# Optimization experiments

Measured on AMD Instinct MI355X. Metric: run time of the kernel, lower is better.

## Reference

```python
import jax, jax.numpy as jnp
import numpy as np

SEQ = 4096
E = 2048

def setup_inputs() -> dict:
    key = jax.random.key(0)
    kx, kq, kk, kv = jax.random.split(key, 4)
    scale = 1.0 / np.sqrt(E)
    x = jax.random.normal(kx, (SEQ, E), dtype=jnp.float32)
    # nn.Linear weights: shape [out, in], applied as x @ W.T
    Wq = jax.random.uniform(kq, (E, E), dtype=jnp.float32, minval=-scale, maxval=scale)
    Wk = jax.random.uniform(kk, (E, E), dtype=jnp.float32, minval=-scale, maxval=scale)
    Wv = jax.random.uniform(kv, (E, E), dtype=jnp.float32, minval=-scale, maxval=scale)
    return {"x": x, "Wq": Wq, "Wk": Wk, "Wv": Wv}

def reference(x, Wq, Wk, Wv):
    # q/k/v projections: nn.Linear(bias=False) -> x @ W.T
    q = x @ Wq.T  # [S, E]
    k = x @ Wk.T  # [S, E]
    v = x @ Wv.T  # [S, E]
    s = q @ k.T  # [S, S]
    w = jax.nn.softmax(s / jnp.sqrt(jnp.float32(E)), axis=-1)
    return w @ v  # [S, E]
```

## Files before the change

### kernel.cpp

```cpp
#include <hip/hip_runtime.h>
#include <hip/hip_bf16.h>

#define S_DIM 4096
#define E_DIM 2048

typedef __attribute__((ext_vector_type(4))) float f32x4;
typedef __attribute__((ext_vector_type(8))) short bf16x8;

__device__ __forceinline__ unsigned short f2bf(float f) {
  unsigned u = __builtin_bit_cast(unsigned, f);
  u += 0x7FFFu + ((u >> 16) & 1u);
  return (unsigned short)(u >> 16);
}
__device__ __forceinline__ float bf2f(unsigned short h) {
  return __builtin_bit_cast(float, ((unsigned)h) << 16);
}

__global__ __launch_bounds__(256) void cast_kernel(const float* __restrict__ in,
                                                   unsigned short* __restrict__ out,
                                                   int n4) {
  int i = blockIdx.x * 256 + threadIdx.x;
  if (i >= n4) return;
  float4 v = reinterpret_cast<const float4*>(in)[i];
  ushort4 o;
  o.x = f2bf(v.x); o.y = f2bf(v.y); o.z = f2bf(v.z); o.w = f2bf(v.w);
  reinterpret_cast<ushort4*>(out)[i] = o;
}

__global__ __launch_bounds__(256) void cast3_kernel(const float* __restrict__ w0,
                                                    const float* __restrict__ w1,
                                                    const float* __restrict__ w2,
                                                    unsigned short* __restrict__ out,
                                                    int n4each) {
  int i = blockIdx.x * 256 + threadIdx.x;
  if (i >= 3 * n4each) return;
  const float* src = (i < n4each) ? w0 : (i < 2 * n4each ? w1 : w2);
  int j = (i < n4each) ? i : (i < 2 * n4each ? i - n4each : i - 2 * n4each);
  float4 v = reinterpret_cast<const float4*>(src)[j];
  ushort4 o;
  o.x = f2bf(v.x); o.y = f2bf(v.y); o.z = f2bf(v.z); o.w = f2bf(v.w);
  reinterpret_cast<ushort4*>(out)[i] = o;
}

__global__ __launch_bounds__(256) void add_kernel(const float* __restrict__ a,
                                                  const float* __restrict__ b,
                                                  float* __restrict__ o, int n4) {
  int i = blockIdx.x * 256 + threadIdx.x;
  if (i >= n4) return;
  float4 va = reinterpret_cast<const float4*>(a)[i];
  float4 vb = reinterpret_cast<const float4*>(b)[i];
  float4 vo = {va.x + vb.x, va.y + vb.y, va.z + vb.z, va.w + vb.w};
  reinterpret_cast<float4*>(o)[i] = vo;
}


__device__ __forceinline__ void stage_half(const unsigned short* __restrict__ g,
                                           int grow0, int ld, int kByte0,
                                           char* ldsHalfBase, int tid) {
#pragma unroll
  for (int p = 0; p < 2; ++p) {
    const int o = (p * 512 + tid) * 16;
    const int S = o >> 10;
    const int oi = o & 1023;
    const int osi = oi ^ (((oi >> 9) & 1) << 5);
    const int r  = (S >> 1) * 16 + (osi >> 6);
    const int cb = (S & 1) * 64 + (osi & 63);
    const char* ga = reinterpret_cast<const char*>(g) +
                     ((size_t)(grow0 + r) * ld) * 2 + kByte0 + cb;
    char* la = ldsHalfBase + (o & ~1023);
    __builtin_amdgcn_global_load_lds(
        (const __attribute__((address_space(1))) void*)ga,
        (__attribute__((address_space(3))) void*)la, 16, 0, 0);
  }
}

#define MFMA_QUAD(AM, AN, AF, BF)                                              \
  _Pragma("unroll") for (int mm = 0; mm < 4; ++mm)                             \
  _Pragma("unroll") for (int nn = 0; nn < 2; ++nn)                             \
  _Pragma("unroll") for (int ks = 0; ks < 2; ++ks)                             \
    acc[(AM) + mm][(AN) + nn] = __builtin_amdgcn_mfma_f32_16x16x32_bf16(       \
        AF[mm][ks], BF[nn][ks], acc[(AM) + mm][(AN) + nn], 0, 0, 0);

enum { EPI_QKV = 0, EPI_BF16 = 1, EPI_F32 = 2 };

template <int EPI>
__global__ __launch_bounds__(512, 2) void gemm8(
    const unsigned short* __restrict__ A, const unsigned short* __restrict__ B,
    int lda, int ldb, int K,
    float* __restrict__ Cf, unsigned short* __restrict__ Cb,
    unsigned short* __restrict__ Ct, int ldc, float scale,
    int kElemPerZ, long long zStrideC) {
  extern __shared__ char lds[];

  const int tid = threadIdx.x;
  int bx = blockIdx.x, by = blockIdx.y;
  {
    const int gx = gridDim.x;
    const int nwg = gx * gridDim.y;
    const int orig = by * gx + bx;
    const int q = nwg >> 3;
    const int s = (orig & 7) * q + (orig >> 3);
    bx = s % gx; by = s / gx;
  }
  const int rowA0 = by * 256;
  const int rowB0 = bx * 256;
  const int k0B = blockIdx.z * kElemPerZ * 2;
  if (EPI == EPI_F32) Cf += (size_t)blockIdx.z * zStrideC;

  const int wave = tid >> 6;
  const int lane = tid & 63;
  const int wm = wave >> 2;
  const int wn = wave & 3;
  const int l15 = lane & 15;
  const int kg = lane >> 4;
  const int rsw = (l15 * 64 + kg * 16) ^ ((l15 & 8) << 2);

  int bSub[2][2];
#pragma unroll
  for (int nh = 0; nh < 2; ++nh)
#pragma unroll
    for (int nn = 0; nn < 2; ++nn) {
      const int row = wn * 64 + nh * 32 + nn * 16;
      bSub[nh][nn] = 32768 + (row >> 7) * 16384 + ((row & 127) >> 4) * 2048;
    }
  const int aBase = wm * 16384;

  f32x4 acc[8][4];
#pragma unroll
  for (int mi = 0; mi < 8; ++mi)
#pragma unroll
    for (int ni = 0; ni < 4; ++ni) acc[mi][ni] = (f32x4){0.f, 0.f, 0.f, 0.f};

  const int NT = K / 64;
  char* buf0 = lds;
  char* buf1 = lds + 65536;

  stage_half(A, rowA0,       lda, k0B,       buf0 + 0,     tid);
  stage_half(A, rowA0 + 128, lda, k0B,       buf0 + 16384, tid);
  stage_half(B, rowB0,       ldb, k0B,       buf0 + 32768, tid);
  stage_half(B, rowB0 + 128, ldb, k0B,       buf0 + 49152, tid);
  stage_half(B, rowB0,       ldb, k0B + 128, buf1 + 32768, tid);
  stage_half(B, rowB0 + 128, ldb, k0B + 128, buf1 + 49152, tid);
  stage_half(A, rowA0,       lda, k0B + 128, buf1 + 0,     tid);
  stage_half(A, rowA0 + 128, lda, k0B + 128, buf1 + 16384, tid);
  asm volatile("s_waitcnt vmcnt(8)" ::: "memory");
  __builtin_amdgcn_sched_barrier(0);
  __builtin_amdgcn_s_barrier();

  for (int t = 0; t < NT; ++t) {
    char* bufc = lds + (t & 1) * 65536;
    bf16x8 a0[4][2], a1[4][2], b0[2][2], b1[2][2];

#pragma unroll
    for (int mm = 0; mm < 4; ++mm)
#pragma unroll
      for (int ks = 0; ks < 2; ++ks)
        a0[mm][ks] = *reinterpret_cast<const bf16x8*>(
            bufc + aBase + (mm * 2 + ks) * 1024 + rsw);
#pragma unroll
    for (int nn = 0; nn < 2; ++nn)
#pragma unroll
      for (int ks = 0; ks < 2; ++ks)
        b0[nn][ks] = *reinterpret_cast<const bf16x8*>(
            bufc + bSub[0][nn] + ks * 1024 + rsw);
    asm volatile("s_waitcnt lgkmcnt(8)" ::: "memory");
    __builtin_amdgcn_s_barrier();
    asm volatile("s_waitcnt lgkmcnt(0)" ::: "memory");
    __builtin_amdgcn_sched_barrier(0);
    __builtin_amdgcn_s_setprio(1);
    MFMA_QUAD(0, 0, a0, b0)
    __builtin_amdgcn_s_setprio(0);
    __builtin_amdgcn_s_barrier();

#pragma unroll
    for (int nn = 0; nn < 2; ++nn)
#pragma unroll
      for (int ks = 0; ks < 2; ++ks)
        b1[nn][ks] = *reinterpret_cast<const bf16x8*>(
            bufc + bSub[1][nn] + ks * 1024 + rsw);
    __builtin_amdgcn_s_barrier();
    asm volatile("s_waitcnt lgkmcnt(0)" ::: "memory");
    __builtin_amdgcn_sched_barrier(0);
    __builtin_amdgcn_s_setprio(1);
    MFMA_QUAD(0, 2, a0, b1)
    __builtin_amdgcn_s_setprio(0);
    __builtin_amdgcn_s_barrier();

#pragma unroll
    for (int mm = 0; mm < 4; ++mm)
#pragma unroll
      for (int ks = 0; ks < 2; ++ks)
        a1[mm][ks] = *reinterpret_cast<const bf16x8*>(
            bufc + aBase + ((4 + mm) * 2 + ks) * 1024 + rsw);
    if (t + 2 < NT) {
      const int kb = k0B + (t + 2) * 128;
      stage_half(B, rowB0,       ldb, kb, bufc + 32768, tid);
      stage_half(B, rowB0 + 128, ldb, kb, bufc + 49152, tid);
    }
    __builtin_amdgcn_s_barrier();
    asm volatile("s_waitcnt lgkmcnt(0)" ::: "memory");
    __builtin_amdgcn_sched_barrier(0);
    __builtin_amdgcn_s_setprio(1);
    MFMA_QUAD(4, 2, a1, b1)
    __builtin_amdgcn_s_setprio(0);
    __builtin_amdgcn_s_barrier();

    if (t + 2 < NT) {
      const int kb = k0B + (t + 2) * 128;
      stage_half(A, rowA0,       lda, kb, bufc + 0,     tid);
      stage_half(A, rowA0 + 128, lda, kb, bufc + 16384, tid);
      asm volatile("s_waitcnt vmcnt(8)" ::: "memory");
    } else {
      asm volatile("s_waitcnt vmcnt(0)" ::: "memory");
    }
    __builtin_amdgcn_sched_barrier(0);
    __builtin_amdgcn_s_barrier();
    __builtin_amdgcn_s_setprio(1);
    MFMA_QUAD(4, 0, a1, b0)
    __builtin_amdgcn_s_setprio(0);
    __builtin_amdgcn_s_barrier();
  }

  const int r0 = rowA0 + wm * 128;
  const int c0 = rowB0 + wn * 64;
#pragma unroll
  for (int mi = 0; mi < 8; ++mi) {
    const int row = r0 + (mi >> 2) * 64 + (mi & 3) * 16 + kg * 4;
#pragma unroll
    for (int ni = 0; ni < 4; ++ni) {
      const int col = c0 + (ni >> 1) * 32 + (ni & 1) * 16 + l15;
      f32x4 v = acc[mi][ni];
      if constexpr (EPI == EPI_F32) {
#pragma unroll
        for (int r = 0; r < 4; ++r)
          Cf[(size_t)(row + r) * ldc + col] = v[r];
      } else if constexpr (EPI == EPI_BF16) {
#pragma unroll
        for (int r = 0; r < 4; ++r)
          Cb[(size_t)(row + r) * ldc + col] = f2bf(v[r] * scale);
      } else {
        if (rowB0 < 4096) {
#pragma unroll
          for (int r = 0; r < 4; ++r)
            Cb[(size_t)(row + r) * 4096 + col] = f2bf(v[r]);
        } else {
          ushort4 pk;
          pk.x = f2bf(v[0]); pk.y = f2bf(v[1]);
          pk.z = f2bf(v[2]); pk.w = f2bf(v[3]);
          *reinterpret_cast<ushort4*>(Ct + (size_t)(col - 4096) * 4096 + row) = pk;
        }
      }
    }
  }
}

__global__ __launch_bounds__(256) void softmax_kernel(const unsigned short* __restrict__ Sm,
                                                      unsigned short* __restrict__ P) {
  const int row = blockIdx.x;
  const int tid = threadIdx.x;
  const unsigned short* src = Sm + (size_t)row * S_DIM;
  float vals[16];
  float mx = -1e30f;
#pragma unroll
  for (int i = 0; i < 4; ++i) {
    ushort4 h = reinterpret_cast<const ushort4*>(src)[tid + i * 256];
    float a = bf2f(h.x), b = bf2f(h.y), c = bf2f(h.z), d = bf2f(h.w);
    vals[i * 4 + 0] = a; vals[i * 4 + 1] = b;
    vals[i * 4 + 2] = c; vals[i * 4 + 3] = d;
    mx = fmaxf(mx, fmaxf(fmaxf(a, b), fmaxf(c, d)));
  }
#pragma unroll
  for (int off = 32; off >= 1; off >>= 1) mx = fmaxf(mx, __shfl_xor(mx, off, 64));
  __shared__ float red[8];
  const int wave = tid >> 6, lane = tid & 63;
  if (lane == 0) red[wave] = mx;
  __syncthreads();
  mx = fmaxf(fmaxf(red[0], red[1]), fmaxf(red[2], red[3]));
  float sum = 0.f;
#pragma unroll
  for (int i = 0; i < 16; ++i) { vals[i] = __expf(vals[i] - mx); sum += vals[i]; }
#pragma unroll
  for (int off = 32; off >= 1; off >>= 1) sum += __shfl_xor(sum, off, 64);
  if (lane == 0) red[4 + wave] = sum;
  __syncthreads();
  sum = red[4] + red[5] + red[6] + red[7];
  const float inv = 1.0f / sum;
  unsigned short* dst = P + (size_t)row * S_DIM;
#pragma unroll
  for (int i = 0; i < 4; ++i) {
    ushort4 pk;
    pk.x = f2bf(vals[i * 4 + 0] * inv);
    pk.y = f2bf(vals[i * 4 + 1] * inv);
    pk.z = f2bf(vals[i * 4 + 2] * inv);
    pk.w = f2bf(vals[i * 4 + 3] * inv);
    reinterpret_cast<ushort4*>(dst)[tid + i * 256] = pk;
  }
}

extern "C" void kernel_launch(void* const* d_in, const int* in_sizes, int n_in,
                              void* d_out, int out_size, void* d_ws, size_t ws_size,
                              hipStream_t stream) {
  const float* x  = (const float*)d_in[0];
  const float* Wq = (const float*)d_in[1];
  const float* Wk = (const float*)d_in[2];
  const float* Wv = (const float*)d_in[3];
  float* out = (float*)d_out;
  char* ws = (char*)d_ws;

  const size_t MB = 1024 * 1024;
  const size_t NEED = 120 * MB;
  if (ws_size < NEED) return;

  unsigned short* xb   = (unsigned short*)(ws);
  unsigned short* wcat = (unsigned short*)(ws + 16 * MB);
  unsigned short* qkb  = (unsigned short*)(ws + 40 * MB);
  unsigned short* vt   = (unsigned short*)(ws + 72 * MB);
  unsigned short* Sb   = (unsigned short*)(ws + 88 * MB);
  float* outp0 = (float*)(ws);
  float* outp1 = (float*)(ws + 88 * MB);
  unsigned short* P = qkb;

  hipFuncSetAttribute(reinterpret_cast<const void*>(&gemm8<EPI_QKV>),
                      hipFuncAttributeMaxDynamicSharedMemorySize, 131072);
  hipFuncSetAttribute(reinterpret_cast<const void*>(&gemm8<EPI_BF16>),
                      hipFuncAttributeMaxDynamicSharedMemorySize, 131072);
  hipFuncSetAttribute(reinterpret_cast<const void*>(&gemm8<EPI_F32>),
                      hipFuncAttributeMaxDynamicSharedMemorySize, 131072);

  const int nx4 = S_DIM * E_DIM / 4;
  const int nw4 = E_DIM * E_DIM / 4;

  cast_kernel<<<nx4 / 256, 256, 0, stream>>>(x, xb, nx4);
  cast3_kernel<<<3 * nw4 / 256, 256, 0, stream>>>(Wq, Wk, Wv, wcat, nw4);

  gemm8<EPI_QKV><<<dim3(24, 16, 1), 512, 131072, stream>>>(
      xb, wcat, E_DIM, E_DIM, E_DIM, nullptr, qkb, vt, 4096, 1.0f, 0, 0);

  const float scale = 0.022097086912079608f;
  gemm8<EPI_BF16><<<dim3(16, 16, 1), 512, 131072, stream>>>(
      qkb, qkb + 2048, 4096, 4096, E_DIM, nullptr, Sb, nullptr, 4096, scale, 0, 0);

  softmax_kernel<<<S_DIM, 256, 0, stream>>>(Sb, P);

  gemm8<EPI_F32><<<dim3(8, 16, 2), 512, 131072, stream>>>(
      P, vt, 4096, 4096, 2048, outp0, nullptr, nullptr, E_DIM, 1.0f,
      2048, (long long)(88 * MB) / 4);

  add_kernel<<<nx4 / 256, 256, 0, stream>>>(outp0, outp1, out, nx4);
}
```

Before: 404.4 us.

## Software-pipeline LDS fragment reads across MFMA quadrants and drop XCD workgroup remap

```diff
diff --git a/kernel.cpp b/kernel.cpp
--- a/kernel.cpp
+++ b/kernel.cpp
@@ -81,6 +81,24 @@
     acc[(AM) + mm][(AN) + nn] = __builtin_amdgcn_mfma_f32_16x16x32_bf16(       \
         AF[mm][ks], BF[nn][ks], acc[(AM) + mm][(AN) + nn], 0, 0, 0);
 
+#define READ_A0(dst, buf)                                                      \
+  _Pragma("unroll") for (int mm = 0; mm < 4; ++mm)                             \
+  _Pragma("unroll") for (int ks = 0; ks < 2; ++ks)                             \
+    dst[mm][ks] = *reinterpret_cast<const bf16x8*>(                            \
+        (buf) + aBase + (mm * 2 + ks) * 1024 + rsw);
+
+#define READ_A1(dst, buf)                                                      \
+  _Pragma("unroll") for (int mm = 0; mm < 4; ++mm)                             \
+  _Pragma("unroll") for (int ks = 0; ks < 2; ++ks)                             \
+    dst[mm][ks] = *reinterpret_cast<const bf16x8*>(                            \
+        (buf) + aBase + ((4 + mm) * 2 + ks) * 1024 + rsw);
+
+#define READ_B(dst, buf, nh)                                                   \
+  _Pragma("unroll") for (int nn = 0; nn < 2; ++nn)                             \
+  _Pragma("unroll") for (int ks = 0; ks < 2; ++ks)                             \
+    dst[nn][ks] = *reinterpret_cast<const bf16x8*>(                            \
+        (buf) + bSub[nh][nn] + ks * 1024 + rsw);
+
 enum { EPI_QKV = 0, EPI_BF16 = 1, EPI_F32 = 2 };
 
 template <int EPI>
@@ -93,17 +111,8 @@
   extern __shared__ char lds[];
 
   const int tid = threadIdx.x;
-  int bx = blockIdx.x, by = blockIdx.y;
-  {
-    const int gx = gridDim.x;
-    const int nwg = gx * gridDim.y;
-    const int orig = by * gx + bx;
-    const int q = nwg >> 3;
-    const int s = (orig & 7) * q + (orig >> 3);
-    bx = s % gx; by = s / gx;
-  }
-  const int rowA0 = by * 256;
-  const int rowB0 = bx * 256;
+  const int rowA0 = blockIdx.y * 256;
+  const int rowB0 = blockIdx.x * 256;
   const int k0B = blockIdx.z * kElemPerZ * 2;
   if (EPI == EPI_F32) Cf += (size_t)blockIdx.z * zStrideC;
 
@@ -139,64 +148,50 @@
   stage_half(A, rowA0 + 128, lda, k0B,       buf0 + 16384, tid);
   stage_half(B, rowB0,       ldb, k0B,       buf0 + 32768, tid);
   stage_half(B, rowB0 + 128, ldb, k0B,       buf0 + 49152, tid);
+  stage_half(A, rowA0,       lda, k0B + 128, buf1 + 0,     tid);
+  stage_half(A, rowA0 + 128, lda, k0B + 128, buf1 + 16384, tid);
   stage_half(B, rowB0,       ldb, k0B + 128, buf1 + 32768, tid);
   stage_half(B, rowB0 + 128, ldb, k0B + 128, buf1 + 49152, tid);
-  stage_half(A, rowA0,       lda, k0B + 128, buf1 + 0,     tid);
-  stage_half(A, rowA0 + 128, lda, k0B + 128, buf1 + 16384, tid);
   asm volatile("s_waitcnt vmcnt(8)" ::: "memory");
   __builtin_amdgcn_sched_barrier(0);
   __builtin_amdgcn_s_barrier();
 
+  bf16x8 a0[4][2], a1[4][2], b0[2][2], b1[2][2];
+  READ_A0(a0, buf0)
+  READ_B(b0, buf0, 0)
+  __builtin_amdgcn_sched_barrier(0);
+
   for (int t = 0; t < NT; ++t) {
     char* bufc = lds + (t & 1) * 65536;
-    bf16x8 a0[4][2], a1[4][2], b0[2][2], b1[2][2];
-
-#pragma unroll
-    for (int mm = 0; mm < 4; ++mm)
-#pragma unroll
-      for (int ks = 0; ks < 2; ++ks)
-        a0[mm][ks] = *reinterpret_cast<const bf16x8*>(
-            bufc + aBase + (mm * 2 + ks) * 1024 + rsw);
-#pragma unroll
-    for (int nn = 0; nn < 2; ++nn)
-#pragma unroll
-      for (int ks = 0; ks < 2; ++ks)
-        b0[nn][ks] = *reinterpret_cast<const bf16x8*>(
-            bufc + bSub[0][nn] + ks * 1024 + rsw);
-    asm volatile("s_waitcnt lgkmcnt(8)" ::: "memory");
-    __builtin_amdgcn_s_barrier();
-    asm volatile("s_waitcnt lgkmcnt(0)" ::: "memory");
+    char* bufn = lds + ((t & 1) ^ 1) * 65536;
+
+    READ_B(b1, bufc, 1)
+    __builtin_amdgcn_s_barrier();
+    asm volatile("s_waitcnt lgkmcnt(4)" ::: "memory");
     __builtin_amdgcn_sched_barrier(0);
     __builtin_amdgcn_s_setprio(1);
     MFMA_QUAD(0, 0, a0, b0)
     __builtin_amdgcn_s_setprio(0);
     __builtin_amdgcn_s_barrier();
 
-#pragma unroll
-    for (int nn = 0; nn < 2; ++nn)
-#pragma unroll
-      for (int ks = 0; ks < 2; ++ks)
-        b1[nn][ks] = *reinterpret_cast<const bf16x8*>(
-            bufc + bSub[1][nn] + ks * 1024 + rsw);
-    __builtin_amdgcn_s_barrier();
-    asm volatile("s_waitcnt lgkmcnt(0)" ::: "memory");
+    READ_A1(a1, bufc)
+    __builtin_amdgcn_s_barrier();
+    asm volatile("s_waitcnt lgkmcnt(8)" ::: "memory");
     __builtin_amdgcn_sched_barrier(0);
     __builtin_amdgcn_s_setprio(1);
     MFMA_QUAD(0, 2, a0, b1)
     __builtin_amdgcn_s_setprio(0);
     __builtin_amdgcn_s_barrier();
 
-#pragma unroll
-    for (int mm = 0; mm < 4; ++mm)
-#pragma unroll
-      for (int ks = 0; ks < 2; ++ks)
-        a1[mm][ks] = *reinterpret_cast<const bf16x8*>(
-            bufc + aBase + ((4 + mm) * 2 + ks) * 1024 + rsw);
     if (t + 2 < NT) {
       const int kb = k0B + (t + 2) * 128;
       stage_half(B, rowB0,       ldb, kb, bufc + 32768, tid);
       stage_half(B, rowB0 + 128, ldb, kb, bufc + 49152, tid);
+      asm volatile("s_waitcnt vmcnt(4)" ::: "memory");
+    } else if (t + 1 < NT) {
+      asm volatile("s_waitcnt vmcnt(0)" ::: "memory");
     }
+    __builtin_amdgcn_sched_barrier(0);
     __builtin_amdgcn_s_barrier();
     asm volatile("s_waitcnt lgkmcnt(0)" ::: "memory");
     __builtin_amdgcn_sched_barrier(0);
@@ -205,19 +200,20 @@
     __builtin_amdgcn_s_setprio(0);
     __builtin_amdgcn_s_barrier();
 
+    if (t + 1 < NT) { READ_A0(a0, bufn) }
     if (t + 2 < NT) {
       const int kb = k0B + (t + 2) * 128;
       stage_half(A, rowA0,       lda, kb, bufc + 0,     tid);
       stage_half(A, rowA0 + 128, lda, kb, bufc + 16384, tid);
-      asm volatile("s_waitcnt vmcnt(8)" ::: "memory");
-    } else {
-      asm volatile("s_waitcnt vmcnt(0)" ::: "memory");
     }
     __builtin_amdgcn_sched_barrier(0);
     __builtin_amdgcn_s_barrier();
     __builtin_amdgcn_s_setprio(1);
     MFMA_QUAD(4, 0, a1, b0)
     __builtin_amdgcn_s_setprio(0);
+    __builtin_amdgcn_sched_barrier(0);
+    if (t + 1 < NT) { READ_B(b0, bufn, 0) }
+    __builtin_amdgcn_sched_barrier(0);
     __builtin_amdgcn_s_barrier();
   }
 
```

After: 403.5 us. Within noise of the previous version (-0.2%).

## Replace 256x256 8-wave GEMM with 128x128 4-wave tile, drop split-K

Applied to the files above, without the earlier changes.

```diff
diff --git a/kernel.cpp b/kernel.cpp
--- a/kernel.cpp
+++ b/kernel.cpp
@@ -42,24 +42,12 @@
   reinterpret_cast<ushort4*>(out)[i] = o;
 }
 
-__global__ __launch_bounds__(256) void add_kernel(const float* __restrict__ a,
-                                                  const float* __restrict__ b,
-                                                  float* __restrict__ o, int n4) {
-  int i = blockIdx.x * 256 + threadIdx.x;
-  if (i >= n4) return;
-  float4 va = reinterpret_cast<const float4*>(a)[i];
-  float4 vb = reinterpret_cast<const float4*>(b)[i];
-  float4 vo = {va.x + vb.x, va.y + vb.y, va.z + vb.z, va.w + vb.w};
-  reinterpret_cast<float4*>(o)[i] = vo;
-}
-
-
-__device__ __forceinline__ void stage_half(const unsigned short* __restrict__ g,
-                                           int grow0, int ld, int kByte0,
-                                           char* ldsHalfBase, int tid) {
-#pragma unroll
-  for (int p = 0; p < 2; ++p) {
-    const int o = (p * 512 + tid) * 16;
+__device__ __forceinline__ void stage_half128(const unsigned short* __restrict__ g,
+                                              int grow0, int ld, int kByte0,
+                                              char* base, int tid) {
+#pragma unroll
+  for (int p = 0; p < 4; ++p) {
+    const int o = (p * 256 + tid) * 16;
     const int S = o >> 10;
     const int oi = o & 1023;
     const int osi = oi ^ (((oi >> 9) & 1) << 5);
@@ -67,168 +55,115 @@
     const int cb = (S & 1) * 64 + (osi & 63);
     const char* ga = reinterpret_cast<const char*>(g) +
                      ((size_t)(grow0 + r) * ld) * 2 + kByte0 + cb;
-    char* la = ldsHalfBase + (o & ~1023);
+    char* la = base + (o & ~1023);
     __builtin_amdgcn_global_load_lds(
         (const __attribute__((address_space(1))) void*)ga,
         (__attribute__((address_space(3))) void*)la, 16, 0, 0);
   }
 }
 
-#define MFMA_QUAD(AM, AN, AF, BF)                                              \
-  _Pragma("unroll") for (int mm = 0; mm < 4; ++mm)                             \
-  _Pragma("unroll") for (int nn = 0; nn < 2; ++nn)                             \
-  _Pragma("unroll") for (int ks = 0; ks < 2; ++ks)                             \
-    acc[(AM) + mm][(AN) + nn] = __builtin_amdgcn_mfma_f32_16x16x32_bf16(       \
-        AF[mm][ks], BF[nn][ks], acc[(AM) + mm][(AN) + nn], 0, 0, 0);
 
 enum { EPI_QKV = 0, EPI_BF16 = 1, EPI_F32 = 2 };
 
 template <int EPI>
-__global__ __launch_bounds__(512, 2) void gemm8(
+__global__ __launch_bounds__(256, 2) void gemm128(
     const unsigned short* __restrict__ A, const unsigned short* __restrict__ B,
     int lda, int ldb, int K,
     float* __restrict__ Cf, unsigned short* __restrict__ Cb,
-    unsigned short* __restrict__ Ct, int ldc, float scale,
-    int kElemPerZ, long long zStrideC) {
+    unsigned short* __restrict__ Ct, int ldc, float scale) {
   extern __shared__ char lds[];
 
   const int tid = threadIdx.x;
-  int bx = blockIdx.x, by = blockIdx.y;
-  {
-    const int gx = gridDim.x;
-    const int nwg = gx * gridDim.y;
-    const int orig = by * gx + bx;
-    const int q = nwg >> 3;
-    const int s = (orig & 7) * q + (orig >> 3);
-    bx = s % gx; by = s / gx;
-  }
-  const int rowA0 = by * 256;
-  const int rowB0 = bx * 256;
-  const int k0B = blockIdx.z * kElemPerZ * 2;
-  if (EPI == EPI_F32) Cf += (size_t)blockIdx.z * zStrideC;
+  const int rowA0 = blockIdx.y * 128;
+  const int rowB0 = blockIdx.x * 128;
 
   const int wave = tid >> 6;
   const int lane = tid & 63;
-  const int wm = wave >> 2;
-  const int wn = wave & 3;
+  const int wm = wave >> 1;
+  const int wn = wave & 1;
   const int l15 = lane & 15;
   const int kg = lane >> 4;
   const int rsw = (l15 * 64 + kg * 16) ^ ((l15 & 8) << 2);
-
-  int bSub[2][2];
-#pragma unroll
-  for (int nh = 0; nh < 2; ++nh)
-#pragma unroll
-    for (int nn = 0; nn < 2; ++nn) {
-      const int row = wn * 64 + nh * 32 + nn * 16;
-      bSub[nh][nn] = 32768 + (row >> 7) * 16384 + ((row & 127) >> 4) * 2048;
-    }
-  const int aBase = wm * 16384;
-
-  f32x4 acc[8][4];
-#pragma unroll
-  for (int mi = 0; mi < 8; ++mi)
+  const int aBase = wm * 8192;
+  const int bBase = 16384 + wn * 8192;
+
+  f32x4 acc[4][4];
+#pragma unroll
+  for (int mi = 0; mi < 4; ++mi)
 #pragma unroll
     for (int ni = 0; ni < 4; ++ni) acc[mi][ni] = (f32x4){0.f, 0.f, 0.f, 0.f};
 
   const int NT = K / 64;
   char* buf0 = lds;
-  char* buf1 = lds + 65536;
-
-  stage_half(A, rowA0,       lda, k0B,       buf0 + 0,     tid);
-  stage_half(A, rowA0 + 128, lda, k0B,       buf0 + 16384, tid);
-  stage_half(B, rowB0,       ldb, k0B,       buf0 + 32768, tid);
-  stage_half(B, rowB0 + 128, ldb, k0B,       buf0 + 49152, tid);
-  stage_half(B, rowB0,       ldb, k0B + 128, buf1 + 32768, tid);
-  stage_half(B, rowB0 + 128, ldb, k0B + 128, buf1 + 49152, tid);
-  stage_half(A, rowA0,       lda, k0B + 128, buf1 + 0,     tid);
-  stage_half(A, rowA0 + 128, lda, k0B + 128, buf1 + 16384, tid);
+  char* buf1 = lds + 32768;
+
+  stage_half128(A, rowA0, lda, 0,   buf0 + 0,     tid);
+  stage_half128(B, rowB0, ldb, 0,   buf0 + 16384, tid);
+  stage_half128(A, rowA0, lda, 128, buf1 + 0,     tid);
+  stage_half128(B, rowB0, ldb, 128, buf1 + 16384, tid);
   asm volatile("s_waitcnt vmcnt(8)" ::: "memory");
   __builtin_amdgcn_sched_barrier(0);
   __builtin_amdgcn_s_barrier();
 
   for (int t = 0; t < NT; ++t) {
-    char* bufc = lds + (t & 1) * 65536;
-    bf16x8 a0[4][2], a1[4][2], b0[2][2], b1[2][2];
+    char* bufc = lds + (t & 1) * 32768;
+    bf16x8 af[4][2], bf[4][2];
 
 #pragma unroll
     for (int mm = 0; mm < 4; ++mm)
 #pragma unroll
       for (int ks = 0; ks < 2; ++ks)
-        a0[mm][ks] = *reinterpret_cast<const bf16x8*>(
+        af[mm][ks] = *reinterpret_cast<const bf16x8*>(
             bufc + aBase + (mm * 2 + ks) * 1024 + rsw);
 #pragma unroll
-    for (int nn = 0; nn < 2; ++nn)
+    for (int nn = 0; nn < 4; ++nn)
 #pragma unroll
       for (int ks = 0; ks < 2; ++ks)
-        b0[nn][ks] = *reinterpret_cast<const bf16x8*>(
-            bufc + bSub[0][nn] + ks * 1024 + rsw);
-    asm volatile("s_waitcnt lgkmcnt(8)" ::: "memory");
+        bf[nn][ks] = *reinterpret_cast<const bf16x8*>(
+            bufc + bBase + (nn * 2 + ks) * 1024 + rsw);
+    __builtin_amdgcn_sched_barrier(0);
     __builtin_amdgcn_s_barrier();
     asm volatile("s_waitcnt lgkmcnt(0)" ::: "memory");
     __builtin_amdgcn_sched_barrier(0);
     __builtin_amdgcn_s_setprio(1);
-    MFMA_QUAD(0, 0, a0, b0)
+#pragma unroll
+    for (int mm = 0; mm < 4; ++mm)
+#pragma unroll
+      for (int nn = 0; nn < 4; ++nn)
+        acc[mm][nn] = __builtin_amdgcn_mfma_f32_16x16x32_bf16(
+            af[mm][0], bf[nn][0], acc[mm][nn], 0, 0, 0);
     __builtin_amdgcn_s_setprio(0);
     __builtin_amdgcn_s_barrier();
 
-#pragma unroll
-    for (int nn = 0; nn < 2; ++nn)
-#pragma unroll
-      for (int ks = 0; ks < 2; ++ks)
-        b1[nn][ks] = *reinterpret_cast<const bf16x8*>(
-            bufc + bSub[1][nn] + ks * 1024 + rsw);
-    __builtin_amdgcn_s_barrier();
-    asm volatile("s_waitcnt lgkmcnt(0)" ::: "memory");
-    __builtin_amdgcn_sched_barrier(0);
-    __builtin_amdgcn_s_setprio(1);
-    MFMA_QUAD(0, 2, a0, b1)
-    __builtin_amdgcn_s_setprio(0);
-    __builtin_amdgcn_s_barrier();
-
-#pragma unroll
-    for (int mm = 0; mm < 4; ++mm)
-#pragma unroll
-      for (int ks = 0; ks < 2; ++ks)
-        a1[mm][ks] = *reinterpret_cast<const bf16x8*>(
-            bufc + aBase + ((4 + mm) * 2 + ks) * 1024 + rsw);
     if (t + 2 < NT) {
-      const int kb = k0B + (t + 2) * 128;
-      stage_half(B, rowB0,       ldb, kb, bufc + 32768, tid);
-      stage_half(B, rowB0 + 128, ldb, kb, bufc + 49152, tid);
-    }
-    __builtin_amdgcn_s_barrier();
-    asm volatile("s_waitcnt lgkmcnt(0)" ::: "memory");
-    __builtin_amdgcn_sched_barrier(0);
-    __builtin_amdgcn_s_setprio(1);
-    MFMA_QUAD(4, 2, a1, b1)
-    __builtin_amdgcn_s_setprio(0);
-    __builtin_amdgcn_s_barrier();
-
-    if (t + 2 < NT) {
-      const int kb = k0B + (t + 2) * 128;
-      stage_half(A, rowA0,       lda, kb, bufc + 0,     tid);
-      stage_half(A, rowA0 + 128, lda, kb, bufc + 16384, tid);
+      const int kb = (t + 2) * 128;
+      stage_half128(A, rowA0, lda, kb, bufc + 0,     tid);
+      stage_half128(B, rowB0, ldb, kb, bufc + 16384, tid);
       asm volatile("s_waitcnt vmcnt(8)" ::: "memory");
     } else {
       asm volatile("s_waitcnt vmcnt(0)" ::: "memory");
     }
     __builtin_amdgcn_sched_barrier(0);
+    __builtin_amdgcn_s_setprio(1);
+#pragma unroll
+    for (int mm = 0; mm < 4; ++mm)
+#pragma unroll
+      for (int nn = 0; nn < 4; ++nn)
+        acc[mm][nn] = __builtin_amdgcn_mfma_f32_16x16x32_bf16(
+            af[mm][1], bf[nn][1], acc[mm][nn], 0, 0, 0);
+    __builtin_amdgcn_s_setprio(0);
+    __builtin_amdgcn_sched_barrier(0);
     __builtin_amdgcn_s_barrier();
-    __builtin_amdgcn_s_setprio(1);
-    MFMA_QUAD(4, 0, a1, b0)
-    __builtin_amdgcn_s_setprio(0);
-    __builtin_amdgcn_s_barrier();
-  }
-
-  const int r0 = rowA0 + wm * 128;
+  }
+
+  const int r0 = rowA0 + wm * 64;
   const int c0 = rowB0 + wn * 64;
 #pragma unroll
-  for (int mi = 0; mi < 8; ++mi) {
-    const int row = r0 + (mi >> 2) * 64 + (mi & 3) * 16 + kg * 4;
+  for (int mi = 0; mi < 4; ++mi) {
+    const int row = r0 + mi * 16 + kg * 4;
 #pragma unroll
     for (int ni = 0; ni < 4; ++ni) {
-      const int col = c0 + (ni >> 1) * 32 + (ni & 1) * 16 + l15;
+      const int col = c0 + ni * 16 + l15;
       f32x4 v = acc[mi][ni];
       if constexpr (EPI == EPI_F32) {
 #pragma unroll
@@ -316,16 +251,14 @@
   unsigned short* qkb  = (unsigned short*)(ws + 40 * MB);
   unsigned short* vt   = (unsigned short*)(ws + 72 * MB);
   unsigned short* Sb   = (unsigned short*)(ws + 88 * MB);
-  float* outp0 = (float*)(ws);
-  float* outp1 = (float*)(ws + 88 * MB);
   unsigned short* P = qkb;
 
-  hipFuncSetAttribute(reinterpret_cast<const void*>(&gemm8<EPI_QKV>),
-                      hipFuncAttributeMaxDynamicSharedMemorySize, 131072);
-  hipFuncSetAttribute(reinterpret_cast<const void*>(&gemm8<EPI_BF16>),
-                      hipFuncAttributeMaxDynamicSharedMemorySize, 131072);
-  hipFuncSetAttribute(reinterpret_cast<const void*>(&gemm8<EPI_F32>),
-                      hipFuncAttributeMaxDynamicSharedMemorySize, 131072);
+  hipFuncSetAttribute(reinterpret_cast<const void*>(&gemm128<EPI_QKV>),
+                      hipFuncAttributeMaxDynamicSharedMemorySize, 65536);
+  hipFuncSetAttribute(reinterpret_cast<const void*>(&gemm128<EPI_BF16>),
+                      hipFuncAttributeMaxDynamicSharedMemorySize, 65536);
+  hipFuncSetAttribute(reinterpret_cast<const void*>(&gemm128<EPI_F32>),
+                      hipFuncAttributeMaxDynamicSharedMemorySize, 65536);
 
   const int nx4 = S_DIM * E_DIM / 4;
   const int nw4 = E_DIM * E_DIM / 4;
@@ -333,18 +266,15 @@
   cast_kernel<<<nx4 / 256, 256, 0, stream>>>(x, xb, nx4);
   cast3_kernel<<<3 * nw4 / 256, 256, 0, stream>>>(Wq, Wk, Wv, wcat, nw4);
 
-  gemm8<EPI_QKV><<<dim3(24, 16, 1), 512, 131072, stream>>>(
-      xb, wcat, E_DIM, E_DIM, E_DIM, nullptr, qkb, vt, 4096, 1.0f, 0, 0);
+  gemm128<EPI_QKV><<<dim3(48, 32), 256, 65536, stream>>>(
+      xb, wcat, E_DIM, E_DIM, E_DIM, nullptr, qkb, vt, 4096, 1.0f);
 
   const float scale = 0.022097086912079608f;
-  gemm8<EPI_BF16><<<dim3(16, 16, 1), 512, 131072, stream>>>(
-      qkb, qkb + 2048, 4096, 4096, E_DIM, nullptr, Sb, nullptr, 4096, scale, 0, 0);
+  gemm128<EPI_BF16><<<dim3(32, 32), 256, 65536, stream>>>(
+      qkb, qkb + 2048, 4096, 4096, E_DIM, nullptr, Sb, nullptr, 4096, scale);
 
   softmax_kernel<<<S_DIM, 256, 0, stream>>>(Sb, P);
 
-  gemm8<EPI_F32><<<dim3(8, 16, 2), 512, 131072, stream>>>(
-      P, vt, 4096, 4096, 2048, outp0, nullptr, nullptr, E_DIM, 1.0f,
-      2048, (long long)(88 * MB) / 4);
-
-  add_kernel<<<nx4 / 256, 256, 0, stream>>>(outp0, outp1, out, nx4);
-}
+  gemm128<EPI_F32><<<dim3(16, 32), 256, 65536, stream>>>(
+      P, vt, 4096, 4096, S_DIM, out, nullptr, nullptr, E_DIM, 1.0f);
+}
```

Result: no change. 400.0 us (-1.1%).
